# Kernel optimization log

Measured on AMD Instinct MI355X. Metric: run time of the kernel, lower is better.

The kernel has to match this reference:

```python
import jax, jax.numpy as jnp
import numpy as np

D_MODEL = 1024
N_HEADS = 16
D_FF = 4096
EPS = 1e-5


def _linear_init(key, fan_in, fan_out):
    # torch nn.Linear default: U(-1/sqrt(fan_in), 1/sqrt(fan_in))
    k1, k2 = jax.random.split(key)
    bound = 1.0 / np.sqrt(fan_in)
    W = jax.random.uniform(k1, (fan_in, fan_out), minval=-bound, maxval=bound, dtype=jnp.float32)
    b = jax.random.uniform(k2, (fan_out,), minval=-bound, maxval=bound, dtype=jnp.float32)
    return W, b


def setup_inputs() -> dict:
    key = jax.random.key(0)
    ks = jax.random.split(key, 8)
    x = jax.random.normal(ks[0], (4, 2048, D_MODEL), dtype=jnp.float32)
    Wq, bq = _linear_init(ks[1], D_MODEL, D_MODEL)
    Wk, bk = _linear_init(ks[2], D_MODEL, D_MODEL)
    Wv, bv = _linear_init(ks[3], D_MODEL, D_MODEL)
    Wo, bo = _linear_init(ks[4], D_MODEL, D_MODEL)
    W1, b1 = _linear_init(ks[5], D_MODEL, D_FF)
    W2, b2 = _linear_init(ks[6], D_FF, D_MODEL)
    g1 = jnp.ones((D_MODEL,), jnp.float32); be1 = jnp.zeros((D_MODEL,), jnp.float32)
    g2 = jnp.ones((D_MODEL,), jnp.float32); be2 = jnp.zeros((D_MODEL,), jnp.float32)
    return {"x": x, "Wq": Wq, "bq": bq, "Wk": Wk, "bk": bk, "Wv": Wv, "bv": bv,
            "Wo": Wo, "bo": bo, "g1": g1, "be1": be1, "W1": W1, "b1": b1,
            "W2": W2, "b2": b2, "g2": g2, "be2": be2}


def _layernorm(x, g, b):
    mu = jnp.mean(x, axis=-1, keepdims=True)
    var = jnp.mean(jnp.square(x - mu), axis=-1, keepdims=True)
    return (x - mu) * jax.lax.rsqrt(var + EPS) * g + b


def reference(x, Wq, bq, Wk, bk, Wv, bv, Wo, bo, g1, be1, W1, b1, W2, b2, g2, be2):
    B, T, D = x.shape
    H, dk = N_HEADS, D // N_HEADS
    # projections -> [B, H, T, dk]
    def split_heads(y):
        return y.reshape(B, T, H, dk).transpose(0, 2, 1, 3)
    Q = split_heads(x @ Wq + bq)
    K = split_heads(x @ Wk + bk)
    V = split_heads(x @ Wv + bv)
    scores = jnp.einsum('bhtd,bhsd->bhts', Q, K) / jnp.sqrt(jnp.float32(dk))
    weights = jax.nn.softmax(scores, axis=-1)  # no causal mask in original
    ctx = jnp.einsum('bhts,bhsd->bhtd', weights, V)
    ctx = ctx.transpose(0, 2, 1, 3).reshape(B, T, D)
    attn_out = ctx @ Wo + bo
    x = _layernorm(x + attn_out, g1, be1)
    ff = jax.nn.relu(x @ W1 + b1) @ W2 + b2
    x = _layernorm(x + ff, g2, be2)
    return x
```

## Files before the change

### kernel.cpp

```cpp
#include <hip/hip_runtime.h>
#include <hip/hip_bf16.h>
#include <stdint.h>

typedef __attribute__((ext_vector_type(8))) short short8;
typedef __attribute__((ext_vector_type(4))) float f32x4;
typedef __attribute__((ext_vector_type(16))) float f32x16;

#define SEQ 2048
#define DMODEL 1024
#define NH 16
#define DKH 64

__device__ __forceinline__ uint16_t f2b(float f) {
  uint32_t u = __float_as_uint(f);
  uint32_t r = (u + 0x7fff + ((u >> 16) & 1)) >> 16;
  return (uint16_t)r;
}
__device__ __forceinline__ float b2f(uint16_t u) {
  return __uint_as_float(((uint32_t)u) << 16);
}

__device__ __forceinline__ void gload16(const uint16_t* g, uint16_t* l) {
  __builtin_amdgcn_global_load_lds((const __attribute__((address_space(1))) void*)g,
                                   (__attribute__((address_space(3))) void*)l, 16, 0, 0);
}

__global__ __launch_bounds__(256) void k_prep(
    const float* __restrict__ Wq, const float* __restrict__ Wk, const float* __restrict__ Wv,
    const float* __restrict__ Wo, const float* __restrict__ W1, const float* __restrict__ W2,
    const float* __restrict__ x, uint16_t* __restrict__ wt_qkv, uint16_t* __restrict__ wt_o,
    uint16_t* __restrict__ wt_1, uint16_t* __restrict__ wt_2, uint16_t* __restrict__ xb) {
  const int id = blockIdx.x;
  if (id >= 12288) {
    int i = (id - 12288) * 256 + threadIdx.x;
    float4 v = reinterpret_cast<const float4*>(x)[i];
    uint16_t o[4] = {f2b(v.x), f2b(v.y), f2b(v.z), f2b(v.w)};
    reinterpret_cast<uint2*>(xb)[i] = *reinterpret_cast<uint2*>(o);
    return;
  }
  __shared__ float tile[32][33];
  const float* W;
  uint16_t* Wt;
  int K, N, bx, by;
  if (id < 4096) {
    int wsel = id >> 10, r = id & 1023;
    K = 1024; N = 1024; bx = r & 31; by = r >> 5;
    W = wsel == 0 ? Wq : (wsel == 1 ? Wk : (wsel == 2 ? Wv : Wo));
    Wt = wsel == 3 ? wt_o : wt_qkv + wsel * 1024 * 1024;
  } else if (id < 8192) {
    int r = id - 4096;
    K = 1024; N = 4096; bx = r & 127; by = r >> 7;
    W = W1; Wt = wt_1;
  } else {
    int r = id - 8192;
    K = 4096; N = 1024; bx = r & 31; by = r >> 5;
    W = W2; Wt = wt_2;
  }
  const int n0 = bx * 32, k0 = by * 32;
  const int tx = threadIdx.x & 31, ty = threadIdx.x >> 5;
#pragma unroll
  for (int i = 0; i < 32; i += 8)
    tile[ty + i][tx] = W[(size_t)(k0 + ty + i) * N + n0 + tx];
  __syncthreads();
#pragma unroll
  for (int i = 0; i < 32; i += 8)
    Wt[(size_t)(n0 + ty + i) * K + k0 + tx] = f2b(tile[tx][ty + i]);
}

__global__ __launch_bounds__(256) void k_vtrans(const uint16_t* __restrict__ V,
                                                uint16_t* __restrict__ Vt) {
  __shared__ uint16_t tile[64][72];
  const int s0 = blockIdx.x * 64;
  const uint16_t* Vp = V + (size_t)blockIdx.y * SEQ * DKH;
  uint16_t* Vtp = Vt + (size_t)blockIdx.y * SEQ * DKH;
  const int t = threadIdx.x;
#pragma unroll
  for (int i = t; i < 512; i += 256) {
    int r = i >> 3, c8 = (i & 7) << 3;
    *reinterpret_cast<uint4*>(&tile[r][c8]) =
        *reinterpret_cast<const uint4*>(Vp + (size_t)(s0 + r) * DKH + c8);
  }
  __syncthreads();
#pragma unroll
  for (int i = t; i < 512; i += 256) {
    int d = i >> 3, s8 = (i & 7) << 3;
    uint16_t tmp[8];
#pragma unroll
    for (int j = 0; j < 8; ++j) tmp[j] = tile[s8 + j][d];
    *reinterpret_cast<uint4*>(Vtp + (size_t)d * SEQ + s0 + s8) = *reinterpret_cast<uint4*>(tmp);
  }
}

#define MODE_QKV 0
#define MODE_RAW 1
#define MODE_RELU 2

template <int BN, int MODE>
__global__ __launch_bounds__(512, 2) void k_gemm2(
    const uint16_t* __restrict__ A, const uint16_t* __restrict__ Bt, int M, int N, int K,
    int nx, const float* __restrict__ bias0, const float* __restrict__ bias1,
    const float* __restrict__ bias2, uint16_t* __restrict__ ob0, uint16_t* __restrict__ ob1,
    uint16_t* __restrict__ ob2, float* __restrict__ of) {
  constexpr int ASZ = 256 * 64;
  constexpr int BSZ = BN * 64;
  __shared__ __align__(16) uint16_t lds[2 * (ASZ + BSZ)];
  uint16_t* const Abase = lds;
  uint16_t* const Bbase = lds + 2 * ASZ;
  constexpr int WN = (BN == 256) ? 4 : 2;
  constexpr int MREP = (BN == 256) ? 8 : 4;
  constexpr int NPH = (BN == 256) ? 4 : 2;
  const int o = blockIdx.x;
  const int chunk = gridDim.x >> 3;
  const int wg = (o & 7) * chunk + (o >> 3);
  const int brow = (wg / nx) << 8;
  const int bcol = (wg % nx) * BN;
  const int t = threadIdx.x;
  const int wid = t >> 6, l = t & 63, g = l >> 4, lr = l & 15;
  const int wr = wid / WN, wc = wid % WN;
  const int wrow = wr * (MREP * 16);
  const int wcol = wc * 64;

  const int srow = t >> 3;
  const int ss0 = (t & 7) ^ (srow & 7);
  const int ss1 = (t & 7) ^ ((srow + 64) & 7);

  auto stage_half = [&](const uint16_t* gsrc, int grow0, int kk, uint16_t* ldst) {
    gload16(gsrc + (size_t)(grow0 + srow) * K + kk + ss0 * 8, ldst + t * 8);
    gload16(gsrc + (size_t)(grow0 + srow + 64) * K + kk + ss1 * 8, ldst + 4096 + t * 8);
  };
  auto rdfrag = [&](const uint16_t* buf, int ar, int kk) -> short8 {
    int slot = ((kk << 2) + g) ^ (ar & 7);
    return *reinterpret_cast<const short8*>(buf + ar * 64 + slot * 8);
  };

  f32x4 acc[MREP][4] = {};
  const int nt = K >> 6;

  stage_half(A, brow, 0, Abase);
  stage_half(A, brow + 128, 0, Abase + 8192);
  stage_half(Bt, bcol, 0, Bbase);
  if (BN == 256) stage_half(Bt, bcol + 128, 0, Bbase + 8192);
  __syncthreads();

  for (int kt = 0; kt < nt; ++kt) {
    const int cur = kt & 1;
    const uint16_t* Ac = Abase + cur * ASZ;
    const uint16_t* Bc = Bbase + cur * BSZ;
    uint16_t* An = Abase + (cur ^ 1) * ASZ;
    uint16_t* Bn = Bbase + (cur ^ 1) * BSZ;
    const bool pf = (kt + 1 < nt);
    const int knx = (kt + 1) << 6;
#pragma unroll
    for (int q = 0; q < NPH; ++q) {
      const int mq = (BN == 256) ? (q >> 1) : 0;
      const int nq = (BN == 256) ? (q & 1) : q;
      short8 af[4][2], bf[2][2];
#pragma unroll
      for (int j = 0; j < 4; ++j)
#pragma unroll
        for (int kk = 0; kk < 2; ++kk)
          af[j][kk] = rdfrag(Ac, wrow + (mq * 4 + j) * 16 + lr, kk);
#pragma unroll
      for (int j = 0; j < 2; ++j)
#pragma unroll
        for (int kk = 0; kk < 2; ++kk)
          bf[j][kk] = rdfrag(Bc, wcol + (nq * 2 + j) * 16 + lr, kk);
      if (pf && q == 0) {
        stage_half(A, brow, knx, An);
        stage_half(A, brow + 128, knx, An + 8192);
        stage_half(Bt, bcol, knx, Bn);
        if (BN == 256) stage_half(Bt, bcol + 128, knx, Bn + 8192);
      }
      __builtin_amdgcn_s_barrier();
      __builtin_amdgcn_s_setprio(1);
#pragma unroll
      for (int j = 0; j < 4; ++j)
#pragma unroll
        for (int j2 = 0; j2 < 2; ++j2)
#pragma unroll
          for (int kk = 0; kk < 2; ++kk)
            acc[mq * 4 + j][nq * 2 + j2] = __builtin_amdgcn_mfma_f32_16x16x32_bf16(
                af[j][kk], bf[j2][kk], acc[mq * 4 + j][nq * 2 + j2], 0, 0, 0);
      __builtin_amdgcn_s_setprio(0);
      if (q == NPH - 1) {
        asm volatile("s_waitcnt vmcnt(0)" ::: "memory");
        __builtin_amdgcn_s_barrier();
        __builtin_amdgcn_sched_barrier(0);
      } else {
        __builtin_amdgcn_s_barrier();
      }
    }
  }

#pragma unroll
  for (int m = 0; m < MREP; ++m) {
#pragma unroll
    for (int n = 0; n < 4; ++n) {
#pragma unroll
      for (int qi = 0; qi < 4; ++qi) {
        int r = brow + wrow + m * 16 + g * 4 + qi;
        int c = bcol + wcol + n * 16 + lr;
        float v = acc[m][n][qi];
        if (MODE == MODE_QKV) {
          int which = c >> 10;
          int hd = c & 1023;
          const float* bp = which == 0 ? bias0 : (which == 1 ? bias1 : bias2);
          v += bp[hd];
          if (which == 0) v *= 0.1803368801f;
          uint16_t* dst = which == 0 ? ob0 : (which == 1 ? ob1 : ob2);
          int b = r >> 11, tt = r & 2047;
          int h = hd >> 6, d = hd & 63;
          dst[((size_t)((b * NH + h) * SEQ + tt)) * DKH + d] = f2b(v);
        } else if (MODE == MODE_RELU) {
          v += bias0[c];
          v = fmaxf(v, 0.0f);
          ob0[(size_t)r * N + c] = f2b(v);
        } else {
          of[(size_t)r * N + c] = v;
        }
      }
    }
  }
}

__global__ __launch_bounds__(256) void k_attn(const uint16_t* __restrict__ Qb,
                                              const uint16_t* __restrict__ Kb,
                                              const uint16_t* __restrict__ Vtg,
                                              uint16_t* __restrict__ ctx) {
  __shared__ __align__(16) uint16_t Ks[2][64 * 64];
  __shared__ __align__(16) uint16_t Vs[2][64 * 64];
  __shared__ float l_arr[4][32];
  const int o = blockIdx.x;
  const int wg = (o & 7) * 128 + (o >> 3);
  const int qt = wg & 15;
  const int bh = wg >> 4;
  const int b = bh >> 4, h = bh & 15;
  const uint16_t* Qp = Qb + (size_t)bh * SEQ * DKH;
  const uint16_t* Kp = Kb + (size_t)bh * SEQ * DKH;
  const uint16_t* Vp = Vtg + (size_t)bh * SEQ * DKH;
  const int t = threadIdx.x, w = t >> 6, l = t & 63;
  const int lo5 = l & 31, hh = l >> 5;
  const int qbase = qt * 128 + w * 32;

  short8 qf[4];
#pragma unroll
  for (int kc = 0; kc < 4; ++kc)
    qf[kc] = *reinterpret_cast<const short8*>(Qp + (size_t)(qbase + lo5) * DKH + kc * 16 + hh * 8);

  f32x16 oacc[2] = {};
  float lsum = 0.f;

  const int swz = ((l & 7) ^ ((l >> 3) & 7)) << 3;
  const int ci0 = w * 2, ci1 = w * 2 + 1;
  const int r0 = ci0 * 8 + (l >> 3), r1 = ci1 * 8 + (l >> 3);
  uint16_t* ldsK0 = &Ks[0][0] + ci0 * 512 + l * 8;
  uint16_t* ldsK1 = &Ks[0][0] + ci1 * 512 + l * 8;
  uint16_t* ldsV0 = &Vs[0][0] + ci0 * 512 + l * 8;
  uint16_t* ldsV1 = &Vs[0][0] + ci1 * 512 + l * 8;
  const uint16_t* gK0 = Kp + (size_t)r0 * DKH + swz;
  const uint16_t* gK1 = Kp + (size_t)r1 * DKH + swz;
  const uint16_t* gV0 = Vp + (size_t)r0 * SEQ + swz;
  const uint16_t* gV1 = Vp + (size_t)r1 * SEQ + swz;

  gload16(gK0, ldsK0);
  gload16(gK1, ldsK1);
  gload16(gV0, ldsV0);
  gload16(gV1, ldsV1);
  __syncthreads();

  for (int tile = 0; tile < 32; ++tile) {
    const int cur = tile & 1;
    if (tile < 31) {
      const int nxt = (cur ^ 1) * 4096;
      const size_t s0n = (size_t)(tile + 1) * 64;
      gload16(gK0 + s0n * DKH, ldsK0 + nxt);
      gload16(gK1 + s0n * DKH, ldsK1 + nxt);
      gload16(gV0 + s0n, ldsV0 + nxt);
      gload16(gV1 + s0n, ldsV1 + nxt);
    }
    const char* Kbuf = reinterpret_cast<const char*>(&Ks[cur][0]);
    const char* Vbuf = reinterpret_cast<const char*>(&Vs[cur][0]);

    short8 kf[2][4];
#pragma unroll
    for (int sblk = 0; sblk < 2; ++sblk) {
      const int krow = sblk * 32 + lo5;
      const int kxor = (krow & 7) << 4;
#pragma unroll
      for (int kc = 0; kc < 4; ++kc) {
        int cb = (kc * 32 + hh * 16) ^ kxor;
        kf[sblk][kc] = *reinterpret_cast<const short8*>(Kbuf + krow * 128 + cb);
      }
    }
    f32x16 sa[2];
#pragma unroll
    for (int sblk = 0; sblk < 2; ++sblk) {
      f32x16 z = {};
      __builtin_amdgcn_s_setprio(1);
#pragma unroll
      for (int kc = 0; kc < 4; ++kc)
        z = __builtin_amdgcn_mfma_f32_32x32x16_bf16(kf[sblk][kc], qf[kc], z, 0, 0, 0);
      __builtin_amdgcn_s_setprio(0);
      sa[sblk] = z;
    }

#pragma unroll
    for (int sblk = 0; sblk < 2; ++sblk) {
      short8 vf[2][2];
#pragma unroll
      for (int scl = 0; scl < 2; ++scl)
#pragma unroll
        for (int dblk = 0; dblk < 2; ++dblk) {
          int vrow = dblk * 32 + lo5;
          int cb = (sblk * 64 + scl * 32 + hh * 16) ^ ((vrow & 7) << 4);
          vf[scl][dblk] = *reinterpret_cast<const short8*>(Vbuf + vrow * 128 + cb);
        }

      float p[16];
      float ls = 0.f;
#pragma unroll
      for (int r = 0; r < 16; ++r) {
        p[r] = __builtin_amdgcn_exp2f(sa[sblk][r]);
        ls += p[r];
      }
      lsum += ls;

      uint32_t clo[4], chi[4];
#pragma unroll
      for (int m = 0; m < 4; ++m) {
        asm("v_cvt_pk_bf16_f32 %0, %1, %2" : "=v"(clo[m]) : "v"(p[4 * m]), "v"(p[4 * m + 1]));
        asm("v_cvt_pk_bf16_f32 %0, %1, %2" : "=v"(chi[m]) : "v"(p[4 * m + 2]), "v"(p[4 * m + 3]));
      }

#pragma unroll
      for (int scl = 0; scl < 2; ++scl) {
        uint32_t a0 = clo[2 * scl], b0 = clo[2 * scl + 1];
        uint32_t a1 = chi[2 * scl], b1 = chi[2 * scl + 1];
        asm("v_permlane32_swap_b32 %0, %1" : "+v"(a0), "+v"(b0));
        asm("v_permlane32_swap_b32 %0, %1" : "+v"(a1), "+v"(b1));
        union {
          uint32_t u[4];
          short8 s;
        } pu;
        pu.u[0] = a0;
        pu.u[1] = a1;
        pu.u[2] = b0;
        pu.u[3] = b1;
        __builtin_amdgcn_s_setprio(1);
#pragma unroll
        for (int dblk = 0; dblk < 2; ++dblk)
          oacc[dblk] = __builtin_amdgcn_mfma_f32_32x32x16_bf16(pu.s, vf[scl][dblk], oacc[dblk], 0, 0, 0);
        __builtin_amdgcn_s_setprio(0);
      }
    }
    __syncthreads();
  }

  {
    float full = lsum + __shfl_xor(lsum, 32, 64);
    if (l < 32) l_arr[w][lo5] = full;
  }
#pragma unroll
  for (int r = 0; r < 16; ++r) {
    int q = (r & 3) + 8 * (r >> 2) + 4 * hh;
    float li = 1.0f / l_arr[w][q];
    int rowg = b * SEQ + qbase + q;
#pragma unroll
    for (int dblk = 0; dblk < 2; ++dblk) {
      int colg = h * DKH + dblk * 32 + lo5;
      ctx[(size_t)rowg * DMODEL + colg] = f2b(oacc[dblk][r] * li);
    }
  }
}

template <bool WRITE_B, bool RESBF>
__global__ __launch_bounds__(256) void k_ln(const float* __restrict__ in,
                                            const float* __restrict__ bias,
                                            const void* __restrict__ res,
                                            const float* __restrict__ gam,
                                            const float* __restrict__ bet,
                                            float* __restrict__ outf,
                                            uint16_t* __restrict__ outb) {
  const int row = blockIdx.x;
  const int t = threadIdx.x, lane = t & 63, w = t >> 6;
  float4 v = reinterpret_cast<const float4*>(in + (size_t)row * DMODEL)[t];
  float4 bb0 = reinterpret_cast<const float4*>(bias)[t];
  float4 rr;
  if (RESBF) {
    uint2 ru = reinterpret_cast<const uint2*>((const uint16_t*)res + (size_t)row * DMODEL)[t];
    const uint16_t* rp = reinterpret_cast<const uint16_t*>(&ru);
    rr.x = b2f(rp[0]);
    rr.y = b2f(rp[1]);
    rr.z = b2f(rp[2]);
    rr.w = b2f(rp[3]);
  } else {
    rr = reinterpret_cast<const float4*>((const float*)res + (size_t)row * DMODEL)[t];
  }
  v.x += bb0.x + rr.x;
  v.y += bb0.y + rr.y;
  v.z += bb0.z + rr.z;
  v.w += bb0.w + rr.w;
  float s = v.x + v.y + v.z + v.w;
  float s2 = v.x * v.x + v.y * v.y + v.z * v.z + v.w * v.w;
#pragma unroll
  for (int off = 1; off < 64; off <<= 1) {
    s += __shfl_xor(s, off, 64);
    s2 += __shfl_xor(s2, off, 64);
  }
  __shared__ float rs[4], rq[4];
  if (lane == 0) {
    rs[w] = s;
    rq[w] = s2;
  }
  __syncthreads();
  float ts = rs[0] + rs[1] + rs[2] + rs[3];
  float tq = rq[0] + rq[1] + rq[2] + rq[3];
  const float inv = 1.0f / DMODEL;
  float mu = ts * inv;
  float var = tq * inv - mu * mu;
  float rstd = rsqrtf(var + 1e-5f);
  float4 gg = reinterpret_cast<const float4*>(gam)[t];
  float4 bb = reinterpret_cast<const float4*>(bet)[t];
  float4 y;
  y.x = (v.x - mu) * rstd * gg.x + bb.x;
  y.y = (v.y - mu) * rstd * gg.y + bb.y;
  y.z = (v.z - mu) * rstd * gg.z + bb.z;
  y.w = (v.w - mu) * rstd * gg.w + bb.w;
  if (WRITE_B) {
    uint16_t oo[4] = {f2b(y.x), f2b(y.y), f2b(y.z), f2b(y.w)};
    reinterpret_cast<uint2*>(outb)[(size_t)row * 256 + t] = *reinterpret_cast<uint2*>(oo);
  } else {
    reinterpret_cast<float4*>(outf)[(size_t)row * 256 + t] = y;
  }
}

extern "C" void kernel_launch(void* const* d_in, const int* in_sizes, int n_in, void* d_out,
                              int out_size, void* d_ws, size_t ws_size, hipStream_t stream) {
  const float* x = (const float*)d_in[0];
  const float* Wq = (const float*)d_in[1];
  const float* bq = (const float*)d_in[2];
  const float* Wk = (const float*)d_in[3];
  const float* bk = (const float*)d_in[4];
  const float* Wv = (const float*)d_in[5];
  const float* bv = (const float*)d_in[6];
  const float* Wo = (const float*)d_in[7];
  const float* bo = (const float*)d_in[8];
  const float* g1 = (const float*)d_in[9];
  const float* be1 = (const float*)d_in[10];
  const float* W1 = (const float*)d_in[11];
  const float* b1 = (const float*)d_in[12];
  const float* W2 = (const float*)d_in[13];
  const float* b2 = (const float*)d_in[14];
  const float* g2 = (const float*)d_in[15];
  const float* be2 = (const float*)d_in[16];

  char* ws = (char*)d_ws;
  size_t off = 0;
  auto alloc = [&](size_t bytes) {
    char* p = ws + off;
    off += (bytes + 255) & ~(size_t)255;
    return p;
  };
  uint16_t* wt_qkv = (uint16_t*)alloc(3072ull * 1024 * 2);
  uint16_t* wt_o = (uint16_t*)alloc(1024ull * 1024 * 2);
  uint16_t* wt_1 = (uint16_t*)alloc(4096ull * 1024 * 2);
  uint16_t* wt_2 = (uint16_t*)alloc(1024ull * 4096 * 2);
  uint16_t* xb = (uint16_t*)alloc(8192ull * 1024 * 2);
  float* sum1 = (float*)alloc(8192ull * 1024 * 4);
  uint16_t* vt = (uint16_t*)alloc(8192ull * 1024 * 2);
  char* big = alloc(16777216ull + 67108864ull);
  uint16_t* Qbuf = (uint16_t*)big;
  uint16_t* Kbuf = (uint16_t*)(big + 16777216ull);
  uint16_t* Vbuf = (uint16_t*)(big + 2 * 16777216ull);
  uint16_t* ctx = xb;
  uint16_t* x1b = (uint16_t*)big;
  uint16_t* hbuf = (uint16_t*)(big + 16777216ull);
  (void)ws_size;

  k_prep<<<20480, 256, 0, stream>>>(Wq, Wk, Wv, Wo, W1, W2, x, wt_qkv, wt_o, wt_1, wt_2, xb);
  k_gemm2<128, MODE_QKV><<<768, 512, 0, stream>>>(
      xb, wt_qkv, 8192, 3072, 1024, 24, bq, bk, bv, Qbuf, Kbuf, Vbuf, nullptr);
  k_vtrans<<<dim3(32, 64), 256, 0, stream>>>(Vbuf, vt);
  k_attn<<<1024, 256, 0, stream>>>(Qbuf, Kbuf, vt, ctx);
  k_gemm2<128, MODE_RAW><<<256, 512, 0, stream>>>(
      ctx, wt_o, 8192, 1024, 1024, 8, nullptr, nullptr, nullptr, nullptr, nullptr, nullptr, sum1);
  k_ln<true, false><<<8192, 256, 0, stream>>>(sum1, bo, x, g1, be1, nullptr, x1b);
  k_gemm2<256, MODE_RELU><<<512, 512, 0, stream>>>(
      x1b, wt_1, 8192, 4096, 1024, 16, b1, nullptr, nullptr, hbuf, nullptr, nullptr, nullptr);
  k_gemm2<128, MODE_RAW><<<256, 512, 0, stream>>>(
      hbuf, wt_2, 8192, 1024, 4096, 8, nullptr, nullptr, nullptr, nullptr, nullptr, nullptr, sum1);
  k_ln<false, true><<<8192, 256, 0, stream>>>(sum1, b2, x1b, g2, be2, (float*)d_out, nullptr);
}
```

Before: 399.0 us.

## Fuse V transpose into QKV GEMM epilogue and store GEMM outputs in bf16

The QKV GEMM epilogue now transposes V tiles through LDS and writes V^T directly, so the separate V-transpose kernel goes away. The output-projection and FFN2 GEMMs write bf16 instead of fp32, and the layernorm reads bf16 inputs, which halves that traffic. The first layernorm now takes its residual from the bf16 copy of x, losing some precision. The attention inner loop is reorganized to compute scores per sub-block, interleaved with the V fragment loads, which lowers register pressure.

Result: faster. 389.3 us (-2.4%).

```diff
diff --git a/kernel.cpp b/kernel.cpp
--- a/kernel.cpp
+++ b/kernel.cpp
@@ -67,32 +67,8 @@
     Wt[(size_t)(n0 + ty + i) * K + k0 + tx] = f2b(tile[tx][ty + i]);
 }
 
-__global__ __launch_bounds__(256) void k_vtrans(const uint16_t* __restrict__ V,
-                                                uint16_t* __restrict__ Vt) {
-  __shared__ uint16_t tile[64][72];
-  const int s0 = blockIdx.x * 64;
-  const uint16_t* Vp = V + (size_t)blockIdx.y * SEQ * DKH;
-  uint16_t* Vtp = Vt + (size_t)blockIdx.y * SEQ * DKH;
-  const int t = threadIdx.x;
-#pragma unroll
-  for (int i = t; i < 512; i += 256) {
-    int r = i >> 3, c8 = (i & 7) << 3;
-    *reinterpret_cast<uint4*>(&tile[r][c8]) =
-        *reinterpret_cast<const uint4*>(Vp + (size_t)(s0 + r) * DKH + c8);
-  }
-  __syncthreads();
-#pragma unroll
-  for (int i = t; i < 512; i += 256) {
-    int d = i >> 3, s8 = (i & 7) << 3;
-    uint16_t tmp[8];
-#pragma unroll
-    for (int j = 0; j < 8; ++j) tmp[j] = tile[s8 + j][d];
-    *reinterpret_cast<uint4*>(Vtp + (size_t)d * SEQ + s0 + s8) = *reinterpret_cast<uint4*>(tmp);
-  }
-}
-
 #define MODE_QKV 0
-#define MODE_RAW 1
+#define MODE_RAWB 1
 #define MODE_RELU 2
 
 template <int BN, int MODE>
@@ -192,6 +168,36 @@
     }
   }
 
+  if (MODE == MODE_QKV && bcol >= 2048) {
+    const int dbase = bcol - 2048;
+#pragma unroll
+    for (int m = 0; m < MREP; ++m) {
+#pragma unroll
+      for (int n = 0; n < 4; ++n) {
+        const int cl = wcol + n * 16 + lr;
+        const float bb = bias2[dbase + cl];
+        uint16_t pk[4];
+#pragma unroll
+        for (int qi = 0; qi < 4; ++qi) pk[qi] = f2b(acc[m][n][qi] + bb);
+        const int r0 = wrow + m * 16 + g * 4;
+        *reinterpret_cast<uint2*>(&lds[cl * 264 + r0]) = *reinterpret_cast<uint2*>(pk);
+      }
+    }
+    __syncthreads();
+    const int bV = brow >> 11;
+    const int tt0 = brow & 2047;
+#pragma unroll
+    for (int j = 0; j < 8; ++j) {
+      int ch = j * 512 + t;
+      int dl = ch >> 5, sc = ch & 31;
+      short8 vv = *reinterpret_cast<const short8*>(&lds[dl * 264 + sc * 8]);
+      int hd = dbase + dl;
+      int h2 = hd >> 6, d = hd & 63;
+      *reinterpret_cast<short8*>(ob2 + ((size_t)(bV * NH + h2)) * SEQ * DKH + (size_t)d * SEQ +
+                                 tt0 + sc * 8) = vv;
+    }
+    return;
+  }
 #pragma unroll
   for (int m = 0; m < MREP; ++m) {
 #pragma unroll
@@ -204,10 +210,10 @@
         if (MODE == MODE_QKV) {
           int which = c >> 10;
           int hd = c & 1023;
-          const float* bp = which == 0 ? bias0 : (which == 1 ? bias1 : bias2);
+          const float* bp = which == 0 ? bias0 : bias1;
           v += bp[hd];
           if (which == 0) v *= 0.1803368801f;
-          uint16_t* dst = which == 0 ? ob0 : (which == 1 ? ob1 : ob2);
+          uint16_t* dst = which == 0 ? ob0 : ob1;
           int b = r >> 11, tt = r & 2047;
           int h = hd >> 6, d = hd & 63;
           dst[((size_t)((b * NH + h) * SEQ + tt)) * DKH + d] = f2b(v);
@@ -216,7 +222,7 @@
           v = fmaxf(v, 0.0f);
           ob0[(size_t)r * N + c] = f2b(v);
         } else {
-          of[(size_t)r * N + c] = v;
+          ob0[(size_t)r * N + c] = f2b(v);
         }
       }
     }
@@ -281,31 +287,16 @@
     const char* Kbuf = reinterpret_cast<const char*>(&Ks[cur][0]);
     const char* Vbuf = reinterpret_cast<const char*>(&Vs[cur][0]);
 
-    short8 kf[2][4];
 #pragma unroll
     for (int sblk = 0; sblk < 2; ++sblk) {
+      short8 kf[4];
       const int krow = sblk * 32 + lo5;
       const int kxor = (krow & 7) << 4;
 #pragma unroll
       for (int kc = 0; kc < 4; ++kc) {
         int cb = (kc * 32 + hh * 16) ^ kxor;
-        kf[sblk][kc] = *reinterpret_cast<const short8*>(Kbuf + krow * 128 + cb);
-      }
-    }
-    f32x16 sa[2];
-#pragma unroll
-    for (int sblk = 0; sblk < 2; ++sblk) {
-      f32x16 z = {};
-      __builtin_amdgcn_s_setprio(1);
-#pragma unroll
-      for (int kc = 0; kc < 4; ++kc)
-        z = __builtin_amdgcn_mfma_f32_32x32x16_bf16(kf[sblk][kc], qf[kc], z, 0, 0, 0);
-      __builtin_amdgcn_s_setprio(0);
-      sa[sblk] = z;
-    }
-
-#pragma unroll
-    for (int sblk = 0; sblk < 2; ++sblk) {
+        kf[kc] = *reinterpret_cast<const short8*>(Kbuf + krow * 128 + cb);
+      }
       short8 vf[2][2];
 #pragma unroll
       for (int scl = 0; scl < 2; ++scl)
@@ -316,11 +307,18 @@
           vf[scl][dblk] = *reinterpret_cast<const short8*>(Vbuf + vrow * 128 + cb);
         }
 
+      f32x16 sa = {};
+      __builtin_amdgcn_s_setprio(1);
+#pragma unroll
+      for (int kc = 0; kc < 4; ++kc)
+        sa = __builtin_amdgcn_mfma_f32_32x32x16_bf16(kf[kc], qf[kc], sa, 0, 0, 0);
+      __builtin_amdgcn_s_setprio(0);
+
       float p[16];
       float ls = 0.f;
 #pragma unroll
       for (int r = 0; r < 16; ++r) {
-        p[r] = __builtin_amdgcn_exp2f(sa[sblk][r]);
+        p[r] = __builtin_amdgcn_exp2f(sa[r]);
         ls += p[r];
       }
       lsum += ls;
@@ -373,8 +371,8 @@
   }
 }
 
-template <bool WRITE_B, bool RESBF>
-__global__ __launch_bounds__(256) void k_ln(const float* __restrict__ in,
+template <bool WRITE_B, bool INBF, bool RESBF>
+__global__ __launch_bounds__(256) void k_ln(const void* __restrict__ in,
                                             const float* __restrict__ bias,
                                             const void* __restrict__ res,
                                             const float* __restrict__ gam,
@@ -383,16 +381,20 @@
                                             uint16_t* __restrict__ outb) {
   const int row = blockIdx.x;
   const int t = threadIdx.x, lane = t & 63, w = t >> 6;
-  float4 v = reinterpret_cast<const float4*>(in + (size_t)row * DMODEL)[t];
+  float4 v;
+  if (INBF) {
+    uint2 iu = reinterpret_cast<const uint2*>((const uint16_t*)in + (size_t)row * DMODEL)[t];
+    const uint16_t* ip = reinterpret_cast<const uint16_t*>(&iu);
+    v.x = b2f(ip[0]); v.y = b2f(ip[1]); v.z = b2f(ip[2]); v.w = b2f(ip[3]);
+  } else {
+    v = reinterpret_cast<const float4*>((const float*)in + (size_t)row * DMODEL)[t];
+  }
   float4 bb0 = reinterpret_cast<const float4*>(bias)[t];
   float4 rr;
   if (RESBF) {
     uint2 ru = reinterpret_cast<const uint2*>((const uint16_t*)res + (size_t)row * DMODEL)[t];
     const uint16_t* rp = reinterpret_cast<const uint16_t*>(&ru);
-    rr.x = b2f(rp[0]);
-    rr.y = b2f(rp[1]);
-    rr.z = b2f(rp[2]);
-    rr.w = b2f(rp[3]);
+    rr.x = b2f(rp[0]); rr.y = b2f(rp[1]); rr.z = b2f(rp[2]); rr.w = b2f(rp[3]);
   } else {
     rr = reinterpret_cast<const float4*>((const float*)res + (size_t)row * DMODEL)[t];
   }
@@ -466,28 +468,26 @@
   uint16_t* wt_1 = (uint16_t*)alloc(4096ull * 1024 * 2);
   uint16_t* wt_2 = (uint16_t*)alloc(1024ull * 4096 * 2);
   uint16_t* xb = (uint16_t*)alloc(8192ull * 1024 * 2);
-  float* sum1 = (float*)alloc(8192ull * 1024 * 4);
+  uint16_t* ctx = (uint16_t*)alloc(8192ull * 1024 * 2);
+  uint16_t* bfout = (uint16_t*)alloc(8192ull * 1024 * 2);
   uint16_t* vt = (uint16_t*)alloc(8192ull * 1024 * 2);
   char* big = alloc(16777216ull + 67108864ull);
   uint16_t* Qbuf = (uint16_t*)big;
   uint16_t* Kbuf = (uint16_t*)(big + 16777216ull);
-  uint16_t* Vbuf = (uint16_t*)(big + 2 * 16777216ull);
-  uint16_t* ctx = xb;
   uint16_t* x1b = (uint16_t*)big;
   uint16_t* hbuf = (uint16_t*)(big + 16777216ull);
   (void)ws_size;
 
   k_prep<<<20480, 256, 0, stream>>>(Wq, Wk, Wv, Wo, W1, W2, x, wt_qkv, wt_o, wt_1, wt_2, xb);
   k_gemm2<128, MODE_QKV><<<768, 512, 0, stream>>>(
-      xb, wt_qkv, 8192, 3072, 1024, 24, bq, bk, bv, Qbuf, Kbuf, Vbuf, nullptr);
-  k_vtrans<<<dim3(32, 64), 256, 0, stream>>>(Vbuf, vt);
+      xb, wt_qkv, 8192, 3072, 1024, 24, bq, bk, bv, Qbuf, Kbuf, vt, nullptr);
   k_attn<<<1024, 256, 0, stream>>>(Qbuf, Kbuf, vt, ctx);
-  k_gemm2<128, MODE_RAW><<<256, 512, 0, stream>>>(
-      ctx, wt_o, 8192, 1024, 1024, 8, nullptr, nullptr, nullptr, nullptr, nullptr, nullptr, sum1);
-  k_ln<true, false><<<8192, 256, 0, stream>>>(sum1, bo, x, g1, be1, nullptr, x1b);
+  k_gemm2<128, MODE_RAWB><<<256, 512, 0, stream>>>(
+      ctx, wt_o, 8192, 1024, 1024, 8, nullptr, nullptr, nullptr, bfout, nullptr, nullptr, nullptr);
+  k_ln<true, true, true><<<8192, 256, 0, stream>>>(bfout, bo, xb, g1, be1, nullptr, x1b);
   k_gemm2<256, MODE_RELU><<<512, 512, 0, stream>>>(
       x1b, wt_1, 8192, 4096, 1024, 16, b1, nullptr, nullptr, hbuf, nullptr, nullptr, nullptr);
-  k_gemm2<128, MODE_RAW><<<256, 512, 0, stream>>>(
-      hbuf, wt_2, 8192, 1024, 4096, 8, nullptr, nullptr, nullptr, nullptr, nullptr, nullptr, sum1);
-  k_ln<false, true><<<8192, 256, 0, stream>>>(sum1, b2, x1b, g2, be2, (float*)d_out, nullptr);
-}
+  k_gemm2<128, MODE_RAWB><<<256, 512, 0, stream>>>(
+      hbuf, wt_2, 8192, 1024, 4096, 8, nullptr, nullptr, nullptr, bfout, nullptr, nullptr, nullptr);
+  k_ln<false, true, true><<<8192, 256, 0, stream>>>(bfout, b2, x1b, g2, be2, (float*)d_out, nullptr);
+}
```
